# Optimization experiments

Hardware: AMD Instinct MI355X
Metric: run time of the kernel (lower is better)

## Reference

```python
import jax, jax.numpy as jnp
from jax import lax
import numpy as np

D = 56      # latent_rep_size
H = 501     # GRU hidden size
T = 277     # repeat length (sequence length)
O = 76      # fc2 output


def setup_inputs() -> dict:
    key = jax.random.key(0)
    ks = jax.random.split(key, 20)
    B = 256
    s = 0.05
    inp = {"x": jax.random.normal(ks[0], (B, D), dtype=jnp.float32)}
    inp["fc1_w"] = jax.random.normal(ks[1], (D, D), dtype=jnp.float32) * s
    inp["fc1_b"] = jax.random.normal(ks[2], (D,), dtype=jnp.float32) * s
    k = 3
    for l, in_dim in enumerate([D, H, H]):
        inp[f"w_ih{l}"] = jax.random.normal(ks[k], (3 * H, in_dim), dtype=jnp.float32) * s; k += 1
        inp[f"w_hh{l}"] = jax.random.normal(ks[k], (3 * H, H), dtype=jnp.float32) * s; k += 1
        inp[f"b_ih{l}"] = jax.random.normal(ks[k], (3 * H,), dtype=jnp.float32) * s; k += 1
        inp[f"b_hh{l}"] = jax.random.normal(ks[k], (3 * H,), dtype=jnp.float32) * s; k += 1
    inp["fc2_w"] = jax.random.normal(ks[k], (O, H), dtype=jnp.float32) * s; k += 1
    inp["fc2_b"] = jax.random.normal(ks[k], (O,), dtype=jnp.float32) * s
    return inp


def _gru_step(h, g, w_hh, b_hh):
    # g: precomputed input gates (B, 3H) in PyTorch order [r, z, n]
    hg = h @ w_hh.T + b_hh                       # (B, 3H)
    r = jax.nn.sigmoid(g[:, :H] + hg[:, :H])
    z = jax.nn.sigmoid(g[:, H:2 * H] + hg[:, H:2 * H])
    n = jnp.tanh(g[:, 2 * H:] + r * hg[:, 2 * H:])
    h_new = (1.0 - z) * n + z * h
    return h_new, h_new


def _gru_layer(x_gates, w_hh, b_hh, B, dtype):
    # x_gates: (T, B, 3H) input contribution per timestep
    h0 = jnp.zeros((B, H), dtype)
    _, ys = lax.scan(lambda h, g: _gru_step(h, g, w_hh, b_hh), h0, x_gates)
    return ys  # (T, B, H)


def reference(x, fc1_w, fc1_b,
              w_ih0, w_hh0, b_ih0, b_hh0,
              w_ih1, w_hh1, b_ih1, b_hh1,
              w_ih2, w_hh2, b_ih2, b_hh2,
              fc2_w, fc2_b):
    B = x.shape[0]
    dtype = x.dtype
    # fc1 + relu, then the input is repeated 277 times -> layer-0 input gates
    # are identical at every timestep; compute them once (B, 3H).
    h_in = jax.nn.relu(x @ fc1_w.T + fc1_b)             # (B, D)
    g0 = h_in @ w_ih0.T + b_ih0                          # (B, 3H), constant over t
    h0 = jnp.zeros((B, H), dtype)
    _, ys0 = lax.scan(lambda h, _: _gru_step(h, g0, w_hh0, b_hh0), h0, None, length=T)
    # layers 1 and 2: precompute input gates for all timesteps, then scan
    g1 = jnp.einsum('tbh,gh->tbg', ys0, w_ih1) + b_ih1   # (T, B, 3H)
    ys1 = _gru_layer(g1, w_hh1, b_hh1, B, dtype)
    g2 = jnp.einsum('tbh,gh->tbg', ys1, w_ih2) + b_ih2
    ys2 = _gru_layer(g2, w_hh2, b_hh2, B, dtype)
    # fc2 then permute(1, 2, 0): (T, B, O) -> (B, O, T)
    out = jnp.einsum('tbh,oh->tbo', ys2, fc2_w) + fc2_b
    return jnp.transpose(out, (1, 2, 0))
```

## Files before the change

kernel.cpp:

```cpp
#include <hip/hip_runtime.h>
#include <hip/hip_bf16.h>
#include <math.h>

#define D_IN 56
#define H    501
#define T_STEPS 277
#define O_OUT 76
#define BATCH 256
#define HP   512
#define NP   1504
#define SSTR 520
#define HSTR 576

#define LDS_SA    0
#define LDS_SB    (32 * SSTR)
#define LDS_SC    (64 * SSTR)
#define LDS_STAGE (96 * SSTR)
#define DYN_LDS   (96 * SSTR * 2 + 18 * HSTR * 4 + 32 * 48 * 4 + 3 * 4 * 16 * 4)

typedef __attribute__((ext_vector_type(8))) short s16x8;
typedef __attribute__((ext_vector_type(4))) float f32x4;
typedef unsigned long long ull;

__device__ __forceinline__ short f2bf(float x) {
    union { float f; unsigned u; } v; v.f = x;
    unsigned r = (v.u + 0x7fffu + ((v.u >> 16) & 1u)) >> 16;
    return (short)r;
}
__device__ __forceinline__ float bf2f(short b) {
    union { unsigned u; float f; } v; v.u = ((unsigned)(unsigned short)b) << 16;
    return v.f;
}
__device__ __forceinline__ float sigm(float x) { return 1.f / (1.f + __expf(-x)); }
__device__ __forceinline__ float tanh_fast(float x) { return 1.f - 2.f / (1.f + __expf(2.f * x)); }

__global__ void k_pack_gru(const float* __restrict__ w_ih,
                           const float* __restrict__ w_hh,
                           short* __restrict__ dst, int KT) {
    int tile = blockIdx.x;
    int ktp  = tile % KT;
    int g    = (tile / KT) % 3;
    int j    = tile / (KT * 3);
    int l    = threadIdx.x;
    int u    = j * 16 + (l & 15);
    int row  = g * H + u;
    const float* src; int k0;
    if (KT == 32) {
        if (ktp < 16) { src = w_ih; k0 = ktp * 32; }
        else          { src = w_hh; k0 = (ktp - 16) * 32; }
    } else          { src = w_hh; k0 = ktp * 32; }
    k0 += (l >> 4) * 8;
    short* p = dst + ((size_t)tile * 64 + l) * 8;
    for (int jj = 0; jj < 8; jj++) {
        int k = k0 + jj;
        float v = 0.f;
        if (u < H && k < H) v = src[(size_t)row * H + k];
        p[jj] = f2bf(v);
    }
}

__global__ void k_pack_fc2(const float* __restrict__ w, short* __restrict__ dst) {
    int tile = blockIdx.x;
    int kt = tile % 16, mt = tile / 16;
    int l = threadIdx.x;
    int o = mt * 16 + (l & 15);
    int k0 = kt * 32 + (l >> 4) * 8;
    short* p = dst + ((size_t)tile * 64 + l) * 8;
    for (int jj = 0; jj < 8; jj++) {
        int k = k0 + jj; float v = 0.f;
        if (o < O_OUT && k < H) v = w[(size_t)o * H + k];
        p[jj] = f2bf(v);
    }
}

__global__ void k_hin(const float* __restrict__ x, const float* __restrict__ w,
                      const float* __restrict__ bias, float* __restrict__ hin) {
    int b = blockIdx.x, o = threadIdx.x;
    float acc = 0.f;
    if (o < D_IN) {
        acc = bias[o];
        for (int k = 0; k < D_IN; k++) acc += x[b * D_IN + k] * w[o * D_IN + k];
        acc = fmaxf(acc, 0.f);
    }
    hin[b * 64 + o] = (o < D_IN) ? acc : 0.f;
}

__global__ void k_g0(const float* __restrict__ hin, const float* __restrict__ w_ih0,
                     const float* __restrict__ b_ih0, float* __restrict__ g0) {
    int b = blockIdx.x, tid = threadIdx.x;
    __shared__ float shx[D_IN];
    if (tid < D_IN) shx[tid] = hin[b * 64 + tid];
    __syncthreads();
    for (int o = tid; o < NP; o += 256) {
        float acc = 0.f;
        if (o < 3 * H) {
            acc = b_ih0[o];
            for (int k = 0; k < D_IN; k++) acc += shx[k] * w_ih0[(size_t)o * D_IN + k];
        }
        g0[(size_t)b * NP + o] = acc;
    }
}

template <int NK>
__device__ __forceinline__ void role_mfma_reg(const short* __restrict__ stg, int abase, int ak0,
                                              const s16x8 (&wv)[48],
                                              float* __restrict__ dr, float* __restrict__ dz,
                                              float* __restrict__ dn, int lane) {
    const int arow = lane & 15;
    const int acol = (lane >> 4) * 8;
    f32x4 ar0 = {0.f,0.f,0.f,0.f}, ar1 = {0.f,0.f,0.f,0.f};
    f32x4 az0 = {0.f,0.f,0.f,0.f}, az1 = {0.f,0.f,0.f,0.f};
    f32x4 an0 = {0.f,0.f,0.f,0.f}, an1 = {0.f,0.f,0.f,0.f};
    #pragma unroll
    for (int kk = 0; kk < NK; kk++) {
        int ak = ak0 + kk;
        s16x8 x0 = *(const s16x8*)&stg[abase + arow * SSTR + ak * 32 + acol];
        s16x8 x1 = *(const s16x8*)&stg[abase + (16 + arow) * SSTR + ak * 32 + acol];
        ar0 = __builtin_amdgcn_mfma_f32_16x16x32_bf16(x0, wv[3 * kk + 0], ar0, 0, 0, 0);
        ar1 = __builtin_amdgcn_mfma_f32_16x16x32_bf16(x1, wv[3 * kk + 0], ar1, 0, 0, 0);
        az0 = __builtin_amdgcn_mfma_f32_16x16x32_bf16(x0, wv[3 * kk + 1], az0, 0, 0, 0);
        az1 = __builtin_amdgcn_mfma_f32_16x16x32_bf16(x1, wv[3 * kk + 1], az1, 0, 0, 0);
        an0 = __builtin_amdgcn_mfma_f32_16x16x32_bf16(x0, wv[3 * kk + 2], an0, 0, 0, 0);
        an1 = __builtin_amdgcn_mfma_f32_16x16x32_bf16(x1, wv[3 * kk + 2], an1, 0, 0, 0);
    }
    int ul = lane & 15, mrow = (lane >> 4) * 4;
    #pragma unroll
    for (int r = 0; r < 4; r++) {
        dr[(mrow + r) * 18 + ul]      = ar0[r];
        dr[(16 + mrow + r) * 18 + ul] = ar1[r];
        dz[(mrow + r) * 18 + ul]      = az0[r];
        dz[(16 + mrow + r) * 18 + ul] = az1[r];
        dn[(mrow + r) * 18 + ul]      = an0[r];
        dn[(16 + mrow + r) * 18 + ul] = an1[r];
    }
}

__global__ __launch_bounds__(384, 2)
void k_gru_persist(const short* __restrict__ packW0,
                   const short* __restrict__ packW1,
                   const short* __restrict__ packW2,
                   const float* __restrict__ g0,
                   const float* __restrict__ b_hh0,
                   const float* __restrict__ b_ih1, const float* __restrict__ b_hh1,
                   const float* __restrict__ b_ih2, const float* __restrict__ b_hh2,
                   short* __restrict__ ysA,
                   short* __restrict__ ysB,
                   unsigned* __restrict__ cnt) {
    const int bg   = blockIdx.x & 7;
    const int j    = blockIdx.x >> 3;
    const int b0   = bg * 32;
    const int tid  = threadIdx.x;
    const int lane = tid & 63;
    const int wave = tid >> 6;
    const s16x8 z8 = {0, 0, 0, 0, 0, 0, 0, 0};

    extern __shared__ __align__(16) char smem[];
    short* stg = (short*)smem;
    float* hgl = (float*)(smem + LDS_STAGE * 2);
    float* sg0 = hgl + 18 * HSTR;
    float* sbb = sg0 + 32 * 48;

    int abase, ak0, slot0;
    s16x8 wv[48];
    {
        const short* wpk; int KT, kt0;
        switch (wave) {
            case 0:  wpk = packW0; KT = 16; kt0 = 0;  abase = LDS_SA; ak0 = 0; slot0 = 0;  break;
            case 1:  wpk = packW0; KT = 16; kt0 = 8;  abase = LDS_SA; ak0 = 8; slot0 = 1;  break;
            case 2:  wpk = packW1; KT = 32; kt0 = 0;  abase = LDS_SA; ak0 = 0; slot0 = 6;  break;
            case 3:  wpk = packW1; KT = 32; kt0 = 16; abase = LDS_SB; ak0 = 0; slot0 = 7;  break;
            case 4:  wpk = packW2; KT = 32; kt0 = 0;  abase = LDS_SB; ak0 = 0; slot0 = 12; break;
            default: wpk = packW2; KT = 32; kt0 = 16; abase = LDS_SC; ak0 = 0; slot0 = 13; break;
        }
        const short* wg0 = wpk + ((size_t)((j * 3 + 0) * KT + kt0) * 512);
        const short* wg1 = wpk + ((size_t)((j * 3 + 1) * KT + kt0) * 512);
        const short* wg2 = wpk + ((size_t)((j * 3 + 2) * KT + kt0) * 512);
        if (wave < 2) {
            #pragma unroll
            for (int kk = 0; kk < 8; kk++) {
                wv[3 * kk + 0] = *(const s16x8*)&wg0[(size_t)kk * 512 + lane * 8];
                wv[3 * kk + 1] = *(const s16x8*)&wg1[(size_t)kk * 512 + lane * 8];
                wv[3 * kk + 2] = *(const s16x8*)&wg2[(size_t)kk * 512 + lane * 8];
            }
        } else {
            #pragma unroll
            for (int kk = 0; kk < 16; kk++) {
                wv[3 * kk + 0] = *(const s16x8*)&wg0[(size_t)kk * 512 + lane * 8];
                wv[3 * kk + 1] = *(const s16x8*)&wg1[(size_t)kk * 512 + lane * 8];
                wv[3 * kk + 2] = *(const s16x8*)&wg2[(size_t)kk * 512 + lane * 8];
            }
        }
    }
    float* dr = hgl + (size_t)slot0 * HSTR;
    float* dz = hgl + (size_t)(slot0 + 2) * HSTR;
    float* dn = hgl + (size_t)(slot0 + 4) * HSTR;

    for (int c = tid; c < 32 * 48; c += 384) {
        int m = c / 48, col = c % 48;
        int g = col >> 4, ul = col & 15;
        int u = j * 16 + ul;
        float v = 0.f;
        if (u < H) {
            v = g0[(size_t)(b0 + m) * NP + g * H + u];
            if (g == 0) v += b_hh0[u];
            else if (g == 1) v += b_hh0[H + u];
        }
        sg0[m * 48 + col] = v;
    }
    if (tid < 48) {
        int l = tid >> 4, ul = tid & 15, u = j * 16 + ul;
        float br = 0.f, bz = 0.f, bxn = 0.f, bhn = 0.f;
        if (u < H) {
            if (l == 0) bhn = b_hh0[2 * H + u];
            else {
                const float* bi = (l == 1) ? b_ih1 : b_ih2;
                const float* bh = (l == 1) ? b_hh1 : b_hh2;
                br = bi[u] + bh[u]; bz = bi[H + u] + bh[H + u];
                bxn = bi[2 * H + u]; bhn = bh[2 * H + u];
            }
        }
        sbb[(l * 4 + 0) * 16 + ul] = br;  sbb[(l * 4 + 1) * 16 + ul] = bz;
        sbb[(l * 4 + 2) * 16 + ul] = bxn; sbb[(l * 4 + 3) * 16 + ul] = bhn;
    }
    __syncthreads();

    unsigned* mycnt = cnt + bg * 32;

    for (int s = 0; s < T_STEPS + 2; ++s) {
        const bool hasL0 = (s < T_STEPS);
        const bool hasL1 = (s >= 1 && s <= T_STEPS);
        const bool hasL2 = (s >= 2);
        const short* ysAm1 = ysA + (size_t)(s - 1) * BATCH * HP;
        const short* ysBm2 = ysB + (size_t)(s - 2) * BATCH * HP;
        const short* ysAm3 = ysA + (size_t)(s - 3) * BATCH * HP;

        #pragma unroll
        for (int i = 0; i < 6; i++) {
            int c = tid + i * 384;
            if (c < 2048) {
                int r = c >> 6, cc = c & 63;
                size_t goff = (size_t)(b0 + r) * HP + cc * 8;
                s16x8 va = z8, vb = z8, vc = z8;
                if (s >= 1 && s <= T_STEPS) va = *(const s16x8*)&ysAm1[goff];
                if (s >= 2)                 vb = *(const s16x8*)&ysBm2[goff];
                if (s >= 3) {
                    const ull* p = (const ull*)&ysAm3[goff];
                    union { ull q[2]; s16x8 v; } uu;
                    uu.q[0] = __hip_atomic_load(p,     __ATOMIC_RELAXED, __HIP_MEMORY_SCOPE_AGENT);
                    uu.q[1] = __hip_atomic_load(p + 1, __ATOMIC_RELAXED, __HIP_MEMORY_SCOPE_AGENT);
                    vc = uu.v;
                }
                int loff = r * SSTR + cc * 8;
                *(s16x8*)&stg[LDS_SA + loff] = va;
                *(s16x8*)&stg[LDS_SB + loff] = vb;
                *(s16x8*)&stg[LDS_SC + loff] = vc;
            }
        }
        __syncthreads();

        {
            const bool active = (wave < 2) ? hasL0 : ((wave < 4) ? hasL1 : hasL2);
            if (active) {
                if (wave < 2) role_mfma_reg<8>(stg, abase, ak0, wv, dr, dz, dn, lane);
                else          role_mfma_reg<16>(stg, abase, ak0, wv, dr, dz, dn, lane);
            }
        }
        __syncthreads();

        #pragma unroll
        for (int it = 0; it < 2; it++) {
            int idx = tid + it * 384;
            int which = idx >> 8, id8 = idx & 255;
            int m = id8 >> 3, pr = id8 & 7;
            int b = b0 + m;
            if (which == 0 && hasL0) {
                short* dst = ysA + (size_t)s * BATCH * HP;
                unsigned pk = 0;
                #pragma unroll
                for (int e = 0; e < 2; e++) {
                    int ul = pr * 2 + e, u = j * 16 + ul, mo = m * 18 + ul;
                    float hv = 0.f;
                    if (u < H) {
                        float hr = hgl[0 * HSTR + mo] + hgl[1 * HSTR + mo];
                        float hz = hgl[2 * HSTR + mo] + hgl[3 * HSTR + mo];
                        float hn = hgl[4 * HSTR + mo] + hgl[5 * HSTR + mo];
                        float r = sigm(sg0[m * 48 + ul] + hr);
                        float z = sigm(sg0[m * 48 + 16 + ul] + hz);
                        float n = tanh_fast(sg0[m * 48 + 32 + ul] + r * (hn + sbb[3 * 16 + ul]));
                        float hold = bf2f(stg[LDS_SA + m * SSTR + u]);
                        hv = (1.f - z) * n + z * hold;
                    }
                    pk |= ((unsigned)(unsigned short)f2bf(hv)) << (16 * e);
                }
                __hip_atomic_store((unsigned*)&dst[(size_t)b * HP + j * 16 + pr * 2], pk,
                                   __ATOMIC_RELAXED, __HIP_MEMORY_SCOPE_AGENT);
            } else if (which == 1 && hasL1) {
                short* dst = ysB + (size_t)(s - 1) * BATCH * HP;
                unsigned pk = 0;
                #pragma unroll
                for (int e = 0; e < 2; e++) {
                    int ul = pr * 2 + e, u = j * 16 + ul, mo = m * 18 + ul;
                    float hv = 0.f;
                    if (u < H) {
                        float xr = hgl[6 * HSTR + mo]  + sbb[(4 + 0) * 16 + ul];
                        float hr = hgl[7 * HSTR + mo];
                        float xz = hgl[8 * HSTR + mo]  + sbb[(4 + 1) * 16 + ul];
                        float hz = hgl[9 * HSTR + mo];
                        float xn = hgl[10 * HSTR + mo] + sbb[(4 + 2) * 16 + ul];
                        float hn = hgl[11 * HSTR + mo] + sbb[(4 + 3) * 16 + ul];
                        float r = sigm(xr + hr);
                        float z = sigm(xz + hz);
                        float n = tanh_fast(xn + r * hn);
                        float hold = bf2f(stg[LDS_SB + m * SSTR + u]);
                        hv = (1.f - z) * n + z * hold;
                    }
                    pk |= ((unsigned)(unsigned short)f2bf(hv)) << (16 * e);
                }
                __hip_atomic_store((unsigned*)&dst[(size_t)b * HP + j * 16 + pr * 2], pk,
                                   __ATOMIC_RELAXED, __HIP_MEMORY_SCOPE_AGENT);
            } else if (which == 2 && hasL2) {
                short* dst = ysA + (size_t)(s - 2) * BATCH * HP;
                unsigned pk = 0;
                #pragma unroll
                for (int e = 0; e < 2; e++) {
                    int ul = pr * 2 + e, u = j * 16 + ul, mo = m * 18 + ul;
                    float hv = 0.f;
                    if (u < H) {
                        float xr = hgl[12 * HSTR + mo] + sbb[(8 + 0) * 16 + ul];
                        float hr = hgl[13 * HSTR + mo];
                        float xz = hgl[14 * HSTR + mo] + sbb[(8 + 1) * 16 + ul];
                        float hz = hgl[15 * HSTR + mo];
                        float xn = hgl[16 * HSTR + mo] + sbb[(8 + 2) * 16 + ul];
                        float hn = hgl[17 * HSTR + mo] + sbb[(8 + 3) * 16 + ul];
                        float r = sigm(xr + hr);
                        float z = sigm(xz + hz);
                        float n = tanh_fast(xn + r * hn);
                        float hold = bf2f(stg[LDS_SC + m * SSTR + u]);
                        hv = (1.f - z) * n + z * hold;
                    }
                    pk |= ((unsigned)(unsigned short)f2bf(hv)) << (16 * e);
                }
                __hip_atomic_store((unsigned*)&dst[(size_t)b * HP + j * 16 + pr * 2], pk,
                                   __ATOMIC_RELAXED, __HIP_MEMORY_SCOPE_AGENT);
            }
        }
        __syncthreads();

        if (tid == 0) {
            asm volatile("s_waitcnt vmcnt(0)" ::: "memory");
            __hip_atomic_fetch_add(mycnt, 1u, __ATOMIC_RELAXED, __HIP_MEMORY_SCOPE_AGENT);
            unsigned tgt = 32u * (unsigned)(s + 1);
            while (__hip_atomic_load(mycnt, __ATOMIC_RELAXED, __HIP_MEMORY_SCOPE_AGENT) < tgt) {}
        }
        __syncthreads();
    }
}

__global__ __launch_bounds__(256, 1)
void k_fc2(const short* __restrict__ ys2, const short* __restrict__ fc2p,
           const float* __restrict__ fc2_b, float* __restrict__ out) {
    int b = blockIdx.x;
    int tid = threadIdx.x, lane = tid & 63, wave = tid >> 6;
    const s16x8 zf = {0, 0, 0, 0, 0, 0, 0, 0};
    for (int ntile = wave; ntile < 18; ntile += 4) {
        int tt = ntile * 16 + (lane & 15);
        s16x8 bf[16];
        for (int kt = 0; kt < 16; kt++) {
            if (tt < T_STEPS)
                bf[kt] = *(const s16x8*)&ys2[((size_t)tt * BATCH + b) * HP + kt * 32 + (lane >> 4) * 8];
            else
                bf[kt] = zf;
        }
        for (int mt = 0; mt < 5; mt++) {
            f32x4 acc = {0.f, 0.f, 0.f, 0.f};
            for (int kt = 0; kt < 16; kt++) {
                s16x8 af = *(const s16x8*)&fc2p[(((size_t)mt * 16 + kt) * 64 + lane) * 8];
                acc = __builtin_amdgcn_mfma_f32_16x16x32_bf16(af, bf[kt], acc, 0, 0, 0);
            }
            int obase = mt * 16 + (lane >> 4) * 4;
            for (int r = 0; r < 4; r++) {
                int o = obase + r;
                if (o < O_OUT && tt < T_STEPS)
                    out[((size_t)b * O_OUT + o) * T_STEPS + tt] = acc[r] + fc2_b[o];
            }
        }
    }
}

extern "C" void kernel_launch(void* const* d_in, const int* in_sizes, int n_in,
                              void* d_out, int out_size, void* d_ws, size_t ws_size,
                              hipStream_t stream) {
    const float* x     = (const float*)d_in[0];
    const float* fc1_w = (const float*)d_in[1];
    const float* fc1_b = (const float*)d_in[2];
    const float* w_ih0 = (const float*)d_in[3];
    const float* w_hh0 = (const float*)d_in[4];
    const float* b_ih0 = (const float*)d_in[5];
    const float* b_hh0 = (const float*)d_in[6];
    const float* w_ih1 = (const float*)d_in[7];
    const float* w_hh1 = (const float*)d_in[8];
    const float* b_ih1 = (const float*)d_in[9];
    const float* b_hh1 = (const float*)d_in[10];
    const float* w_ih2 = (const float*)d_in[11];
    const float* w_hh2 = (const float*)d_in[12];
    const float* b_ih2 = (const float*)d_in[13];
    const float* b_hh2 = (const float*)d_in[14];
    const float* fc2_w = (const float*)d_in[15];
    const float* fc2_b = (const float*)d_in[16];
    float* out = (float*)d_out;

    char* p = (char*)d_ws;
    auto alloc = [&](size_t bytes) {
        char* r = p; p += (bytes + 255) & ~(size_t)255; return r;
    };
    short* packW0 = (short*)alloc((size_t)32 * 3 * 16 * 64 * 8 * 2);
    short* packW1 = (short*)alloc((size_t)32 * 3 * 32 * 64 * 8 * 2);
    short* packW2 = (short*)alloc((size_t)32 * 3 * 32 * 64 * 8 * 2);
    short* packF  = (short*)alloc((size_t)80 * 64 * 8 * 2);
    float* hin    = (float*)alloc((size_t)BATCH * 64 * 4);
    float* g0     = (float*)alloc((size_t)BATCH * NP * 4);
    unsigned* cnt = (unsigned*)alloc(256 * 4);
    short* ysA    = (short*)alloc((size_t)T_STEPS * BATCH * HP * 2);
    short* ysB    = (short*)alloc((size_t)T_STEPS * BATCH * HP * 2);

    static bool attr_set = false;
    if (!attr_set) {
        (void)hipFuncSetAttribute((const void*)k_gru_persist,
                                  hipFuncAttributeMaxDynamicSharedMemorySize,
                                  DYN_LDS);
        attr_set = true;
    }

    hipMemsetAsync(cnt, 0, 256 * 4, stream);
    k_pack_gru<<<32 * 3 * 16, 64, 0, stream>>>(nullptr, w_hh0, packW0, 16);
    k_pack_gru<<<32 * 3 * 32, 64, 0, stream>>>(w_ih1, w_hh1, packW1, 32);
    k_pack_gru<<<32 * 3 * 32, 64, 0, stream>>>(w_ih2, w_hh2, packW2, 32);
    k_pack_fc2<<<80, 64, 0, stream>>>(fc2_w, packF);
    k_hin<<<BATCH, 64, 0, stream>>>(x, fc1_w, fc1_b, hin);
    k_g0<<<BATCH, 256, 0, stream>>>(hin, w_ih0, b_ih0, g0);

    k_gru_persist<<<256, 384, DYN_LDS, stream>>>(packW0, packW1, packW2, g0,
                                                 b_hh0, b_ih1, b_hh1, b_ih2, b_hh2,
                                                 ysA, ysB, cnt);

    k_fc2<<<BATCH, 256, 0, stream>>>(ysA, packF, fc2_b, out);
}
```

Measured before the change: 2.265 ms.

## Use per-block flag barrier and direct global-to-LDS loads in GRU step loop

The grid barrier changes from a shared atomic counter, where every block does fetch_add and then spins, to per-block flags. Each block stores its step number, and 32 lanes poll all flags with a wave-wide __all, which removes contention on one atomic. The per-step staging of the previous hidden states now uses global_load_lds to write straight into LDS, one row per wave, skipping the register round trip and skipping zero-fills for layers that are idle. Weight preloading is rewritten with volatile loads in one unified loop. Flags are read with relaxed ordering, which depends on the existing vmcnt wait for visibility of the data.

```diff
diff --git a/kernel.cpp b/kernel.cpp
--- a/kernel.cpp
+++ b/kernel.cpp
@@ -33,6 +33,12 @@
 }
 __device__ __forceinline__ float sigm(float x) { return 1.f / (1.f + __expf(-x)); }
 __device__ __forceinline__ float tanh_fast(float x) { return 1.f - 2.f / (1.f + __expf(2.f * x)); }
+
+__device__ __forceinline__ void glds16(const void* g, void* l) {
+    __builtin_amdgcn_global_load_lds((const __attribute__((address_space(1))) unsigned int*)g,
+                                     (__attribute__((address_space(3))) unsigned int*)l,
+                                     16, 0, 0);
+}
 
 __global__ void k_pack_gru(const float* __restrict__ w_ih,
                            const float* __restrict__ w_hh,
@@ -172,22 +178,16 @@
             case 4:  wpk = packW2; KT = 32; kt0 = 0;  abase = LDS_SB; ak0 = 0; slot0 = 12; break;
             default: wpk = packW2; KT = 32; kt0 = 16; abase = LDS_SC; ak0 = 0; slot0 = 13; break;
         }
-        const short* wg0 = wpk + ((size_t)((j * 3 + 0) * KT + kt0) * 512);
-        const short* wg1 = wpk + ((size_t)((j * 3 + 1) * KT + kt0) * 512);
-        const short* wg2 = wpk + ((size_t)((j * 3 + 2) * KT + kt0) * 512);
-        if (wave < 2) {
-            #pragma unroll
-            for (int kk = 0; kk < 8; kk++) {
-                wv[3 * kk + 0] = *(const s16x8*)&wg0[(size_t)kk * 512 + lane * 8];
-                wv[3 * kk + 1] = *(const s16x8*)&wg1[(size_t)kk * 512 + lane * 8];
-                wv[3 * kk + 2] = *(const s16x8*)&wg2[(size_t)kk * 512 + lane * 8];
-            }
-        } else {
-            #pragma unroll
-            for (int kk = 0; kk < 16; kk++) {
-                wv[3 * kk + 0] = *(const s16x8*)&wg0[(size_t)kk * 512 + lane * 8];
-                wv[3 * kk + 1] = *(const s16x8*)&wg1[(size_t)kk * 512 + lane * 8];
-                wv[3 * kk + 2] = *(const s16x8*)&wg2[(size_t)kk * 512 + lane * 8];
+        const volatile s16x8* vg0 = (const volatile s16x8*)(wpk + ((size_t)((j * 3 + 0) * KT + kt0) * 512));
+        const volatile s16x8* vg1 = (const volatile s16x8*)(wpk + ((size_t)((j * 3 + 1) * KT + kt0) * 512));
+        const volatile s16x8* vg2 = (const volatile s16x8*)(wpk + ((size_t)((j * 3 + 2) * KT + kt0) * 512));
+        const int NKw = (wave < 2) ? 8 : 16;
+        #pragma unroll
+        for (int kk = 0; kk < 16; kk++) {
+            if (kk < NKw) {
+                wv[3 * kk + 0] = vg0[kk * 64 + lane];
+                wv[3 * kk + 1] = vg1[kk * 64 + lane];
+                wv[3 * kk + 2] = vg2[kk * 64 + lane];
             }
         }
     }
@@ -224,7 +224,7 @@
     }
     __syncthreads();
 
-    unsigned* mycnt = cnt + bg * 32;
+    unsigned* myflags = cnt + bg * 32;
 
     for (int s = 0; s < T_STEPS + 2; ++s) {
         const bool hasL0 = (s < T_STEPS);
@@ -234,28 +234,35 @@
         const short* ysBm2 = ysB + (size_t)(s - 2) * BATCH * HP;
         const short* ysAm3 = ysA + (size_t)(s - 3) * BATCH * HP;
 
-        #pragma unroll
-        for (int i = 0; i < 6; i++) {
-            int c = tid + i * 384;
-            if (c < 2048) {
-                int r = c >> 6, cc = c & 63;
-                size_t goff = (size_t)(b0 + r) * HP + cc * 8;
-                s16x8 va = z8, vb = z8, vc = z8;
-                if (s >= 1 && s <= T_STEPS) va = *(const s16x8*)&ysAm1[goff];
-                if (s >= 2)                 vb = *(const s16x8*)&ysBm2[goff];
-                if (s >= 3) {
-                    const ull* p = (const ull*)&ysAm3[goff];
-                    union { ull q[2]; s16x8 v; } uu;
-                    uu.q[0] = __hip_atomic_load(p,     __ATOMIC_RELAXED, __HIP_MEMORY_SCOPE_AGENT);
-                    uu.q[1] = __hip_atomic_load(p + 1, __ATOMIC_RELAXED, __HIP_MEMORY_SCOPE_AGENT);
-                    vc = uu.v;
+        {
+            const bool needA = (s <= T_STEPS);
+            const bool ldA   = (s >= 1) && needA;
+            const bool needB = hasL1;
+            const bool ldB   = (s >= 2) && needB;
+            const bool needC = hasL2;
+            const bool ldC   = (s >= 3);
+            #pragma unroll
+            for (int i = 0; i < 6; i++) {
+                int r = wave + 6 * i;
+                if (r < 32) {
+                    size_t go = (size_t)(b0 + r) * HP + (size_t)lane * 8;
+                    if (ldA)      glds16(ysAm1 + go, &stg[LDS_SA + r * SSTR]);
+                    else if (needA) *(s16x8*)&stg[LDS_SA + r * SSTR + lane * 8] = z8;
+                    if (ldB)      glds16(ysBm2 + go, &stg[LDS_SB + r * SSTR]);
+                    else if (needB) *(s16x8*)&stg[LDS_SB + r * SSTR + lane * 8] = z8;
+                    if (ldC) {
+                        const ull* pc = (const ull*)(ysAm3 + go);
+                        union { ull q[2]; s16x8 v; } uu;
+                        uu.q[0] = __hip_atomic_load(pc,     __ATOMIC_RELAXED, __HIP_MEMORY_SCOPE_AGENT);
+                        uu.q[1] = __hip_atomic_load(pc + 1, __ATOMIC_RELAXED, __HIP_MEMORY_SCOPE_AGENT);
+                        *(s16x8*)&stg[LDS_SC + r * SSTR + lane * 8] = uu.v;
+                    } else if (needC) {
+                        *(s16x8*)&stg[LDS_SC + r * SSTR + lane * 8] = z8;
+                    }
                 }
-                int loff = r * SSTR + cc * 8;
-                *(s16x8*)&stg[LDS_SA + loff] = va;
-                *(s16x8*)&stg[LDS_SB + loff] = vb;
-                *(s16x8*)&stg[LDS_SC + loff] = vc;
-            }
-        }
+            }
+        }
+        asm volatile("s_waitcnt vmcnt(0)" ::: "memory");
         __syncthreads();
 
         {
@@ -348,9 +355,16 @@
 
         if (tid == 0) {
             asm volatile("s_waitcnt vmcnt(0)" ::: "memory");
-            __hip_atomic_fetch_add(mycnt, 1u, __ATOMIC_RELAXED, __HIP_MEMORY_SCOPE_AGENT);
-            unsigned tgt = 32u * (unsigned)(s + 1);
-            while (__hip_atomic_load(mycnt, __ATOMIC_RELAXED, __HIP_MEMORY_SCOPE_AGENT) < tgt) {}
+            __hip_atomic_store(myflags + j, (unsigned)(s + 1),
+                               __ATOMIC_RELAXED, __HIP_MEMORY_SCOPE_AGENT);
+        }
+        if (tid < 32) {
+            const unsigned tgt = (unsigned)(s + 1);
+            unsigned* fl = myflags + tid;
+            for (;;) {
+                unsigned v = __hip_atomic_load(fl, __ATOMIC_RELAXED, __HIP_MEMORY_SCOPE_AGENT);
+                if (__all(v >= tgt)) break;
+            }
         }
         __syncthreads();
     }
```

New measurement: 2.468 ms. 8.9% more time.
